# Kernel tuning notes

Measured on AMD Instinct MI355X. Metric: run time of the kernel, lower is better.

## Reference

```python
import jax, jax.numpy as jnp
import numpy as np

N, S, M = 16, 256, 768
TK, HA = 10, 1          # tK stages, hA heads (from RTM.__init__)
DH = M // HA
EPS = 1e-5
WSCALE = 0.02           # scale on randn weights to keep 10 stacked stages numerically sane


def _pos_bias():
    # bias[i][j][z] = sin(j / 10000**(2z/M)), bias[i][j][z+1] = cos(...); independent of i
    pos = np.arange(S, dtype=np.float64)[:, None]
    z = np.arange(0, M, 2, dtype=np.float64)
    ang = pos / (10000.0 ** (2.0 * z / M))          # (S, M/2)
    pe = np.zeros((S, M), dtype=np.float32)
    pe[:, 0::2] = np.sin(ang)
    pe[:, 1::2] = np.cos(ang)
    return jnp.asarray(pe)

PE = _pos_bias()


def _ln(v, g, b):
    mu = jnp.mean(v, axis=-1, keepdims=True)
    var = jnp.var(v, axis=-1, keepdims=True)
    return (v - mu) / jnp.sqrt(var + EPS) * g + b


def setup_inputs() -> dict:
    key = jax.random.key(0)
    ks = jax.random.split(key, 8)
    rn = lambda k, shp: jax.random.normal(k, shp, dtype=jnp.float32)
    return {
        "x": rn(ks[0], (N, S, M)),
        "weight": rn(ks[1], (M, M)) * WSCALE,
        "Wq": rn(ks[2], (TK, HA, DH, M)) * WSCALE,
        "Wk": rn(ks[3], (TK, HA, DH, M)) * WSCALE,
        "Wv": rn(ks[4], (TK, HA, DH, M)) * WSCALE,
        "Wo": rn(ks[5], (TK, M, M)) * WSCALE,
        "ln1_g": jnp.ones((M,), jnp.float32), "ln1_b": jnp.zeros((M,), jnp.float32),
        "ln2_g": jnp.ones((M,), jnp.float32), "ln2_b": jnp.zeros((M,), jnp.float32),
        "fc1_w": rn(ks[6], (4 * M, M)) * WSCALE, "fc1_b": jnp.zeros((4 * M,), jnp.float32),
        "fc2_w": rn(ks[7], (M, 4 * M)) * WSCALE, "fc2_b": jnp.zeros((M,), jnp.float32),
    }


def reference(x, weight, Wq, Wk, Wv, Wo, ln1_g, ln1_b, ln2_g, ln2_b,
              fc1_w, fc1_b, fc2_w, fc2_b):
    # savespace[i,j] = weight @ x[i,j,:]  (x[j,:,i] after the double transpose), + sin/cos bias
    s0 = jnp.einsum('mn,ijn->ijm', weight, x) + PE[None, :, :]   # (N, S, M)
    inv_sqrt_dh = jnp.float32(1.0 / np.sqrt(DH))

    def mlp(s):
        h = jax.nn.gelu(s @ fc1_w.T + fc1_b, approximate=False)
        return h @ fc2_w.T + fc2_b

    # Sequential over tokens j: token j attends (strictly causal) to the per-stage V
    # of all previous tokens, accumulated in cumV. Within a token, the tK stages run
    # sequentially, each mutating the token's state s (as the torch code mutates savespace).
    def token_step(cumV, s):                # cumV: (TK, N, HA, DH); s: (N, M)
        newV = []
        for a in range(TK):
            sn = _ln(s, ln1_g, ln1_b)
            q = jnp.einsum('hdm,nm->nhd', Wq[a], sn)
            k = jnp.einsum('hdm,nm->nhd', Wk[a], sn)
            v = jnp.einsum('hdm,nm->nhd', Wv[a], sn)
            logit = jnp.sum(q * inv_sqrt_dh * k, axis=-1)                # (N, HA) scalar score
            rsa = jax.nn.softmax(logit[..., None], axis=-1)[..., 0]      # softmax of scalar == 1
            imv = cumV[a]                                                # (N, HA, DH): sum_{subj<j}
            s = jnp.einsum('mk,nk->nm', Wo[a], imv.reshape(N, HA * DH)) + s
            s = _ln(s, ln2_g, ln2_b) + s
            s = mlp(s)
            newV.append(rsa[..., None] * v)
        return cumV + jnp.stack(newV, axis=0), s

    cumV0 = jnp.zeros((TK, N, HA, DH), x.dtype)
    _, ys = jax.lax.scan(token_step, cumV0, jnp.swapaxes(s0, 0, 1))      # ys: (S, N, M)
    return jnp.swapaxes(ys, 0, 1)                                        # (N, S, M)
```

## Files before the change

kernel.cpp:

```cpp
#include <hip/hip_runtime.h>
#include <hip/hip_bf16.h>
#include <math.h>


using bf16   = __bf16;
using bf16x8 = __attribute__((ext_vector_type(8))) __bf16;
using f32x4  = __attribute__((ext_vector_type(4))) float;

#define DEV __device__ __forceinline__

DEV void gload16(const bf16* g, bf16* l) {
  __builtin_amdgcn_global_load_lds(
      (const __attribute__((address_space(1))) unsigned int*)g,
      (__attribute__((address_space(3))) unsigned int*)l, 16, 0, 0);
}

DEV float gelu_f(float x) {
  const float y  = x * 0.70710678118654752f;
  const float ay = fabsf(y);
  const float t  = __builtin_amdgcn_rcpf(__builtin_fmaf(0.3275911f, ay, 1.0f));
  float p = __builtin_fmaf(1.061405429f, t, -1.453152027f);
  p = __builtin_fmaf(p, t, 1.421413741f);
  p = __builtin_fmaf(p, t, -0.284496736f);
  p = __builtin_fmaf(p, t, 0.254829592f);
  p = p * t;
  const float e = __expf(-ay * ay);
  float er = __builtin_fmaf(-p, e, 1.0f);
  er = __builtin_copysignf(er, y);
  return 0.5f * x * (1.0f + er);
}

enum { EPI_PART = 0, EPI_GELU = 1, EPI_B16 = 2 };

template <int EPI>
__global__ __launch_bounds__(256) void gemm128(
    const bf16* __restrict__ A, const bf16* __restrict__ B,
    float* __restrict__ outF, bf16* __restrict__ outB,
    const float* __restrict__ aux, int K, int N,
    int kZ, int klen, size_t aZ, size_t bZ, size_t oZ)
{
  __shared__ bf16 As[128 * 32];
  __shared__ bf16 Bs[128 * 32];
  const int z = blockIdx.z;
  A += (size_t)z * aZ;
  B += (size_t)z * bZ;
  const int kbeg = z * kZ;
  const int tid  = threadIdx.x;
  const int lane = tid & 63, wave = tid >> 6;
  const int m0 = blockIdx.x * 128, n0 = blockIdx.y * 128;

  const bf16* aG0 = A + (size_t)(m0 + (tid >> 2)) * K + (tid & 3) * 8 + kbeg;
  const bf16* aG1 = aG0 + (size_t)64 * K;
  const bf16* bG0 = B + (size_t)(n0 + (tid >> 2)) * K + (tid & 3) * 8 + kbeg;
  const bf16* bG1 = bG0 + (size_t)64 * K;
  bf16* aL0 = &As[tid * 8];
  bf16* aL1 = &As[2048 + tid * 8];
  bf16* bL0 = &Bs[tid * 8];
  bf16* bL1 = &Bs[2048 + tid * 8];

  const int wr = (wave & 1) * 64, wc = (wave >> 1) * 64;
  const int lr = lane & 15, kb = lane >> 4;
  const bf16* apL = &As[(wr + lr) * 32 + kb * 8];
  const bf16* bpL = &Bs[(wc + lr) * 32 + kb * 8];

  f32x4 acc[4][4] = {};

  for (int k0 = 0; k0 < klen; k0 += 32) {
    gload16(aG0 + k0, aL0);
    gload16(aG1 + k0, aL1);
    gload16(bG0 + k0, bL0);
    gload16(bG1 + k0, bL1);
    __syncthreads();
    bf16x8 af[4], bfv[4];
#pragma unroll
    for (int t = 0; t < 4; ++t) af[t] = *(const bf16x8*)(apL + t * 512);
#pragma unroll
    for (int t = 0; t < 4; ++t) bfv[t] = *(const bf16x8*)(bpL + t * 512);
#pragma unroll
    for (int mt = 0; mt < 4; ++mt)
#pragma unroll
      for (int nt = 0; nt < 4; ++nt)
        acc[mt][nt] = __builtin_amdgcn_mfma_f32_16x16x32_bf16(af[mt], bfv[nt], acc[mt][nt], 0, 0, 0);
    __syncthreads();
  }

  const int row0 = m0 + wr + (lane >> 4) * 4;
  const int col0 = n0 + wc + lr;
  float* oF = (EPI == EPI_PART) ? outF + (size_t)z * oZ : nullptr;
  bf16*  oB = (EPI == EPI_B16)  ? outB + (size_t)z * oZ : outB;
#pragma unroll
  for (int mt = 0; mt < 4; ++mt) {
#pragma unroll
    for (int nt = 0; nt < 4; ++nt) {
      const int col = col0 + nt * 16;
      float bias = 0.f;
      if (EPI == EPI_GELU) bias = aux[col];
#pragma unroll
      for (int r = 0; r < 4; ++r) {
        const int row = row0 + mt * 16 + r;
        float v = acc[mt][nt][r];
        if (EPI == EPI_PART) {
          oF[(size_t)row * N + col] = v;
        } else if (EPI == EPI_GELU) {
          oB[(size_t)row * N + col] = (bf16)gelu_f(v + bias);
        } else {
          oB[(size_t)row * N + col] = (bf16)v;
        }
      }
    }
  }
}

template <int NP, int MODE>
__global__ __launch_bounds__(256) void reduce_ln(
    const float* __restrict__ P, size_t pZ,
    const float* __restrict__ add, const float* __restrict__ g,
    const float* __restrict__ b, float* __restrict__ Tout,
    bf16* __restrict__ SNout)
{
  const int row = blockIdx.x, t = threadIdx.x;
  float v[3];
#pragma unroll
  for (int c = 0; c < 3; ++c) {
    const int col = t + c * 256;
    float s = P[(size_t)row * 768 + col];
#pragma unroll
    for (int p = 1; p < NP; ++p) s += P[(size_t)p * pZ + (size_t)row * 768 + col];
    if (MODE == 0) s += add[(row & 255) * 768 + col];
    if (MODE == 1) s += add[(size_t)row * 768 + col];
    if (MODE == 2 || MODE == 3) s += add[col];
    v[c] = s;
  }
  if (MODE != 1) {
#pragma unroll
    for (int c = 0; c < 3; ++c) Tout[(size_t)row * 768 + t + c * 256] = v[c];
  }
  if (MODE == 3) return;

  __shared__ float red[8];
  float s = v[0] + v[1] + v[2];
#pragma unroll
  for (int o = 32; o >= 1; o >>= 1) s += __shfl_down(s, o);
  if ((t & 63) == 0) red[t >> 6] = s;
  __syncthreads();
  const float mu = (red[0] + red[1] + red[2] + red[3]) * (1.f / 768.f);
  const float d0 = v[0] - mu, d1 = v[1] - mu, d2 = v[2] - mu;
  float q = d0 * d0 + d1 * d1 + d2 * d2;
#pragma unroll
  for (int o = 32; o >= 1; o >>= 1) q += __shfl_down(q, o);
  if ((t & 63) == 0) red[4 + (t >> 6)] = q;
  __syncthreads();
  const float var = (red[4] + red[5] + red[6] + red[7]) * (1.f / 768.f);
  const float rs = rsqrtf(var + 1e-5f);
  float y0 = d0 * rs * g[t] + b[t];
  float y1 = d1 * rs * g[t + 256] + b[t + 256];
  float y2 = d2 * rs * g[t + 512] + b[t + 512];
  if (MODE == 1) { y0 += v[0]; y1 += v[1]; y2 += v[2]; }
  bf16* o = SNout + (size_t)row * 768;
  o[t] = (bf16)y0; o[t + 256] = (bf16)y1; o[t + 512] = (bf16)y2;
}

__global__ __launch_bounds__(256) void scan_partial_b(
    const bf16* __restrict__ SN, float* __restrict__ Ps)
{
  const int n = blockIdx.x, ch = blockIdx.y, d = blockIdx.z * 256 + threadIdx.x;
  const bf16* base = SN + ((size_t)(n * 256 + ch * 16)) * 768 + d;
  float s = 0.f;
#pragma unroll
  for (int j = 0; j < 16; ++j) s += (float)base[(size_t)j * 768];
  Ps[(size_t)(n * 16 + ch) * 768 + d] = s;
}

__global__ __launch_bounds__(256) void scan_final_b(
    const bf16* __restrict__ SN, const float* __restrict__ Ps,
    bf16* __restrict__ PSb)
{
  const int n = blockIdx.x, ch = blockIdx.y, d = blockIdx.z * 256 + threadIdx.x;
  float run = 0.f;
  for (int c = 0; c < ch; ++c) run += Ps[(size_t)(n * 16 + c) * 768 + d];
  const bf16* vb = SN + ((size_t)(n * 256 + ch * 16)) * 768 + d;
  bf16* ob = PSb + ((size_t)(n * 256 + ch * 16)) * 768 + d;
#pragma unroll
  for (int j = 0; j < 16; ++j) {
    ob[(size_t)j * 768] = (bf16)run;
    run += (float)vb[(size_t)j * 768];
  }
}

__global__ __launch_bounds__(256) void transpose_wv(
    const float* __restrict__ Wv, bf16* __restrict__ WvT)
{
  __shared__ float tile[64][65];
  const int a = blockIdx.z, k0 = blockIdx.x * 64, n0 = blockIdx.y * 64;
  const int c = threadIdx.x & 63, r4 = threadIdx.x >> 6;
  const float* src = Wv + (size_t)a * 589824;
  bf16* dst = WvT + (size_t)a * 589824;
#pragma unroll
  for (int i = 0; i < 16; ++i)
    tile[r4 + i * 4][c] = src[(size_t)(k0 + r4 + i * 4) * 768 + n0 + c];
  __syncthreads();
#pragma unroll
  for (int i = 0; i < 16; ++i) {
    const int n = r4 + i * 4;
    dst[(size_t)(n0 + n) * 768 + k0 + c] = (bf16)tile[c][n];
  }
}

__global__ __launch_bounds__(256) void f32_to_bf16_k(
    const float* __restrict__ in, bf16* __restrict__ out, int n4)
{
  const int i = blockIdx.x * 256 + threadIdx.x;
  if (i >= n4) return;
  const float4 v = ((const float4*)in)[i];
  bf16 h[4] = {(bf16)v.x, (bf16)v.y, (bf16)v.z, (bf16)v.w};
  *(uint2*)(out + 4 * (size_t)i) = *(uint2*)h;
}

__global__ __launch_bounds__(256) void pe_kernel(float* __restrict__ PE)
{
  const int id = blockIdx.x * 256 + threadIdx.x;
  const int j = id / 384, p = id % 384;
  const double ang = (double)j * pow(10000.0, -4.0 * (double)p / 768.0);
  PE[(size_t)j * 768 + 2 * p]     = (float)sin(ang);
  PE[(size_t)j * 768 + 2 * p + 1] = (float)cos(ang);
}

extern "C" void kernel_launch(void* const* d_in, const int* in_sizes, int n_in,
                              void* d_out, int out_size, void* d_ws, size_t ws_size,
                              hipStream_t stream)
{
  const float* x      = (const float*)d_in[0];
  const float* weight = (const float*)d_in[1];
  const float* Wv     = (const float*)d_in[4];
  const float* Wo     = (const float*)d_in[5];
  const float* ln1g   = (const float*)d_in[6];
  const float* ln1b   = (const float*)d_in[7];
  const float* ln2g   = (const float*)d_in[8];
  const float* ln2b   = (const float*)d_in[9];
  const float* fc1w   = (const float*)d_in[10];
  const float* fc1b   = (const float*)d_in[11];
  const float* fc2w   = (const float*)d_in[12];
  const float* fc2b   = (const float*)d_in[13];
  float* out = (float*)d_out;

  char* p = (char*)d_ws;
  auto alloc = [&](size_t bytes) { char* r = p; p += (bytes + 255) & ~(size_t)255; return r; };
  bf16*  Wb_w  = (bf16*)alloc(589824ull * 2);
  bf16*  Wb_o  = (bf16*)alloc(5898240ull * 2);
  bf16*  WvT   = (bf16*)alloc(5898240ull * 2);
  bf16*  Wvo   = (bf16*)alloc(5898240ull * 2);
  bf16*  Wb_f1 = (bf16*)alloc(2359296ull * 2);
  bf16*  Wb_f2 = (bf16*)alloc(2359296ull * 2);
  bf16*  Xb    = (bf16*)alloc(3145728ull * 2);
  float* PEf   = (float*)alloc(196608ull * 4);
  float* T     = (float*)alloc(3145728ull * 4);
  bf16*  SN    = (bf16*)alloc(3145728ull * 2);
  bf16*  PSb   = (bf16*)alloc(3145728ull * 2);
  bf16*  H     = (bf16*)alloc(12582912ull * 2);
  float* Ps    = (float*)alloc(196608ull * 4);
  float* Part  = (float*)alloc(2ull * 3145728ull * 4);

  auto cvt = [&](const float* src, bf16* dst, int n) {
    int n4 = n / 4;
    f32_to_bf16_k<<<(n4 + 255) / 256, 256, 0, stream>>>(src, dst, n4);
  };
  cvt(x, Xb, 3145728);
  cvt(weight, Wb_w, 589824);
  cvt(Wo, Wb_o, 5898240);
  cvt(fc1w, Wb_f1, 2359296);
  cvt(fc2w, Wb_f2, 2359296);
  transpose_wv<<<dim3(12, 12, 10), 256, 0, stream>>>(Wv, WvT);
  pe_kernel<<<384, 256, 0, stream>>>(PEf);

  gemm128<EPI_B16><<<dim3(6, 6, 10), 256, 0, stream>>>(
      Wb_o, WvT, nullptr, Wvo, nullptr, 768, 768, 0, 768, 589824, 589824, 589824);

  gemm128<EPI_PART><<<dim3(32, 6, 2), 256, 0, stream>>>(
      Xb, Wb_w, Part, nullptr, nullptr, 768, 768, 384, 384, 0, 0, 3145728);
  reduce_ln<2, 0><<<4096, 256, 0, stream>>>(Part, 3145728, PEf, ln1g, ln1b, T, SN);

  for (int a = 0; a < 10; ++a) {
    scan_partial_b<<<dim3(16, 16, 3), 256, 0, stream>>>(SN, Ps);
    scan_final_b<<<dim3(16, 16, 3), 256, 0, stream>>>(SN, Ps, PSb);
    gemm128<EPI_PART><<<dim3(32, 6, 2), 256, 0, stream>>>(
        PSb, Wvo + (size_t)a * 589824, Part, nullptr, nullptr, 768, 768, 384, 384, 0, 0, 3145728);
    reduce_ln<2, 1><<<4096, 256, 0, stream>>>(Part, 3145728, T, ln2g, ln2b, nullptr, SN);
    gemm128<EPI_GELU><<<dim3(32, 24, 1), 256, 0, stream>>>(
        SN, Wb_f1, nullptr, H, fc1b, 768, 3072, 0, 768, 0, 0, 0);
    gemm128<EPI_PART><<<dim3(32, 6, 2), 256, 0, stream>>>(
        H, Wb_f2, Part, nullptr, nullptr, 3072, 768, 1536, 1536, 0, 0, 3145728);
    if (a < 9)
      reduce_ln<2, 2><<<4096, 256, 0, stream>>>(Part, 3145728, fc2b, ln1g, ln1b, T, SN);
    else
      reduce_ln<2, 3><<<4096, 256, 0, stream>>>(Part, 3145728, fc2b, nullptr, nullptr, out, nullptr);
  }
  (void)in_sizes; (void)n_in; (void)out_size; (void)ws_size;
}
```

Measured before the change: 1.384 ms.

## Double-buffer GEMM LDS tiles, swizzle LDS layout, use 128x64 tiles for narrow GEMMs

After: 1.253 ms. -9.5%, faster.

```diff
diff --git a/kernel.cpp b/kernel.cpp
--- a/kernel.cpp
+++ b/kernel.cpp
@@ -32,56 +32,66 @@
 
 enum { EPI_PART = 0, EPI_GELU = 1, EPI_B16 = 2 };
 
-template <int EPI>
-__global__ __launch_bounds__(256) void gemm128(
+template <int BN, int EPI>
+__global__ __launch_bounds__(256) void gemm_k(
     const bf16* __restrict__ A, const bf16* __restrict__ B,
     float* __restrict__ outF, bf16* __restrict__ outB,
     const float* __restrict__ aux, int K, int N,
     int kZ, int klen, size_t aZ, size_t bZ, size_t oZ)
 {
-  __shared__ bf16 As[128 * 32];
-  __shared__ bf16 Bs[128 * 32];
+  constexpr int ABUF = 128 * 32;
+  constexpr int BBUF = BN * 32;
+  __shared__ bf16 As[2 * ABUF];
+  __shared__ bf16 Bs[2 * BBUF];
   const int z = blockIdx.z;
   A += (size_t)z * aZ;
   B += (size_t)z * bZ;
   const int kbeg = z * kZ;
   const int tid  = threadIdx.x;
   const int lane = tid & 63, wave = tid >> 6;
-  const int m0 = blockIdx.x * 128, n0 = blockIdx.y * 128;
-
-  const bf16* aG0 = A + (size_t)(m0 + (tid >> 2)) * K + (tid & 3) * 8 + kbeg;
+  const int m0 = blockIdx.x * 128, n0 = blockIdx.y * BN;
+
+  const int r  = tid >> 2;
+  const int kq = ((tid & 3) - (tid >> 3)) & 3;
+  const bf16* aG0 = A + (size_t)(m0 + r) * K + kq * 8 + kbeg;
   const bf16* aG1 = aG0 + (size_t)64 * K;
-  const bf16* bG0 = B + (size_t)(n0 + (tid >> 2)) * K + (tid & 3) * 8 + kbeg;
+  const bf16* bG0 = B + (size_t)(n0 + r) * K + kq * 8 + kbeg;
   const bf16* bG1 = bG0 + (size_t)64 * K;
-  bf16* aL0 = &As[tid * 8];
-  bf16* aL1 = &As[2048 + tid * 8];
-  bf16* bL0 = &Bs[tid * 8];
-  bf16* bL1 = &Bs[2048 + tid * 8];
-
-  const int wr = (wave & 1) * 64, wc = (wave >> 1) * 64;
+
+  const int wr = (wave & 1) * 64, wc = (wave >> 1) * (BN / 2);
   const int lr = lane & 15, kb = lane >> 4;
-  const bf16* apL = &As[(wr + lr) * 32 + kb * 8];
-  const bf16* bpL = &Bs[(wc + lr) * 32 + kb * 8];
-
-  f32x4 acc[4][4] = {};
-
-  for (int k0 = 0; k0 < klen; k0 += 32) {
-    gload16(aG0 + k0, aL0);
-    gload16(aG1 + k0, aL1);
-    gload16(bG0 + k0, bL0);
-    gload16(bG1 + k0, bL1);
+  const int swz  = ((kb + (lr >> 1)) & 3) * 8;
+  const int aOff = (wr + lr) * 32 + swz;
+  const int bOff = (wc + lr) * 32 + swz;
+
+  constexpr int MT = 4, NT = BN / 32;
+  f32x4 acc[MT][NT] = {};
+  const int iters = klen >> 5;
+
+  auto stage = [&](int p, int k0) {
+    bf16* aD = &As[p * ABUF + tid * 8];
+    gload16(aG0 + k0, aD);
+    gload16(aG1 + k0, aD + 2048);
+    bf16* bD = &Bs[p * BBUF + tid * 8];
+    gload16(bG0 + k0, bD);
+    if (BN == 128) gload16(bG1 + k0, bD + 2048);
+  };
+
+  stage(0, 0);
+  for (int it = 0; it < iters; ++it) {
     __syncthreads();
-    bf16x8 af[4], bfv[4];
-#pragma unroll
-    for (int t = 0; t < 4; ++t) af[t] = *(const bf16x8*)(apL + t * 512);
-#pragma unroll
-    for (int t = 0; t < 4; ++t) bfv[t] = *(const bf16x8*)(bpL + t * 512);
-#pragma unroll
-    for (int mt = 0; mt < 4; ++mt)
-#pragma unroll
-      for (int nt = 0; nt < 4; ++nt)
+    if (it + 1 < iters) stage((it + 1) & 1, (it + 1) * 32);
+    const int pa = (it & 1) * ABUF, pb = (it & 1) * BBUF;
+    bf16x8 af[MT], bfv[NT];
+#pragma unroll
+    for (int t = 0; t < MT; ++t) af[t] = *(const bf16x8*)&As[pa + aOff + t * 512];
+#pragma unroll
+    for (int t = 0; t < NT; ++t) bfv[t] = *(const bf16x8*)&Bs[pb + bOff + t * 512];
+#pragma unroll
+    for (int mt = 0; mt < MT; ++mt)
+#pragma unroll
+      for (int nt = 0; nt < NT; ++nt)
         acc[mt][nt] = __builtin_amdgcn_mfma_f32_16x16x32_bf16(af[mt], bfv[nt], acc[mt][nt], 0, 0, 0);
-    __syncthreads();
   }
 
   const int row0 = m0 + wr + (lane >> 4) * 4;
@@ -89,16 +99,16 @@
   float* oF = (EPI == EPI_PART) ? outF + (size_t)z * oZ : nullptr;
   bf16*  oB = (EPI == EPI_B16)  ? outB + (size_t)z * oZ : outB;
 #pragma unroll
-  for (int mt = 0; mt < 4; ++mt) {
-#pragma unroll
-    for (int nt = 0; nt < 4; ++nt) {
+  for (int mt = 0; mt < MT; ++mt) {
+#pragma unroll
+    for (int nt = 0; nt < NT; ++nt) {
       const int col = col0 + nt * 16;
       float bias = 0.f;
       if (EPI == EPI_GELU) bias = aux[col];
 #pragma unroll
-      for (int r = 0; r < 4; ++r) {
-        const int row = row0 + mt * 16 + r;
-        float v = acc[mt][nt][r];
+      for (int rg = 0; rg < 4; ++rg) {
+        const int row = row0 + mt * 16 + rg;
+        float v = acc[mt][nt][rg];
         if (EPI == EPI_PART) {
           oF[(size_t)row * N + col] = v;
         } else if (EPI == EPI_GELU) {
@@ -272,22 +282,22 @@
   transpose_wv<<<dim3(12, 12, 10), 256, 0, stream>>>(Wv, WvT);
   pe_kernel<<<384, 256, 0, stream>>>(PEf);
 
-  gemm128<EPI_B16><<<dim3(6, 6, 10), 256, 0, stream>>>(
+  gemm_k<128, EPI_B16><<<dim3(6, 6, 10), 256, 0, stream>>>(
       Wb_o, WvT, nullptr, Wvo, nullptr, 768, 768, 0, 768, 589824, 589824, 589824);
 
-  gemm128<EPI_PART><<<dim3(32, 6, 2), 256, 0, stream>>>(
+  gemm_k<64, EPI_PART><<<dim3(32, 12, 2), 256, 0, stream>>>(
       Xb, Wb_w, Part, nullptr, nullptr, 768, 768, 384, 384, 0, 0, 3145728);
   reduce_ln<2, 0><<<4096, 256, 0, stream>>>(Part, 3145728, PEf, ln1g, ln1b, T, SN);
 
   for (int a = 0; a < 10; ++a) {
     scan_partial_b<<<dim3(16, 16, 3), 256, 0, stream>>>(SN, Ps);
     scan_final_b<<<dim3(16, 16, 3), 256, 0, stream>>>(SN, Ps, PSb);
-    gemm128<EPI_PART><<<dim3(32, 6, 2), 256, 0, stream>>>(
+    gemm_k<64, EPI_PART><<<dim3(32, 12, 2), 256, 0, stream>>>(
         PSb, Wvo + (size_t)a * 589824, Part, nullptr, nullptr, 768, 768, 384, 384, 0, 0, 3145728);
     reduce_ln<2, 1><<<4096, 256, 0, stream>>>(Part, 3145728, T, ln2g, ln2b, nullptr, SN);
-    gemm128<EPI_GELU><<<dim3(32, 24, 1), 256, 0, stream>>>(
+    gemm_k<128, EPI_GELU><<<dim3(32, 24, 1), 256, 0, stream>>>(
         SN, Wb_f1, nullptr, H, fc1b, 768, 3072, 0, 768, 0, 0, 0);
-    gemm128<EPI_PART><<<dim3(32, 6, 2), 256, 0, stream>>>(
+    gemm_k<64, EPI_PART><<<dim3(32, 12, 2), 256, 0, stream>>>(
         H, Wb_f2, Part, nullptr, nullptr, 3072, 768, 1536, 1536, 0, 0, 3145728);
     if (a < 9)
       reduce_ln<2, 2><<<4096, 256, 0, stream>>>(Part, 3145728, fc2b, ln1g, ln1b, T, SN);
```
